# Performance work log

Hardware: AMD Instinct MI355X
Metric: run time of the kernel (lower is better)

The kernel has to match this reference:

```python
import jax, jax.numpy as jnp
import numpy as np

B, S, E, H = 4, 2048, 1024, 16
D = E // H


def setup_inputs() -> dict:
    key = jax.random.key(0)
    ks = jax.random.split(key, 4)
    scale = 0.02
    x = jax.random.normal(ks[0], (B, S, E), dtype=jnp.float32)
    in_proj_w = jax.random.normal(ks[1], (3 * E, E), dtype=jnp.float32) * scale
    in_proj_b = jnp.zeros((3 * E,), dtype=jnp.float32)
    out_w = jax.random.normal(ks[2], (E, E), dtype=jnp.float32) * scale
    out_b = jnp.zeros((E,), dtype=jnp.float32)
    rel_bias = jax.random.normal(ks[3], (2 * 32 + 1, H), dtype=jnp.float32) * 0.02
    return {"x": x, "in_proj_w": in_proj_w, "in_proj_b": in_proj_b,
            "out_w": out_w, "out_b": out_b, "rel_bias": rel_bias,
            "max_rel_dist": 32}


def reference(x, in_proj_w, in_proj_b, out_w, out_b, rel_bias, max_rel_dist):
    b, s, e = x.shape
    h = rel_bias.shape[1]
    d = e // h
    # relative-position indices, clamped: [S, S]
    i = jnp.arange(s)[:, None]
    j = jnp.arange(s)[None, :]
    rel = jnp.clip(i - j, -max_rel_dist, max_rel_dist) + max_rel_dist
    # gather per-pair per-head bias then average over heads -> single 2D mask
    attn_mask = jnp.mean(rel_bias[rel], axis=-1)  # [S, S]
    # fused QKV projection (PyTorch in_proj: x @ W^T + b)
    qkv = x @ in_proj_w.T + in_proj_b           # [B, S, 3E]
    q, k, v = jnp.split(qkv, 3, axis=-1)
    q = q.reshape(b, s, h, d)
    k = k.reshape(b, s, h, d)
    v = v.reshape(b, s, h, d)
    scale = 1.0 / jnp.sqrt(jnp.asarray(d, dtype=x.dtype))
    scores = jnp.einsum('bqhd,bkhd->bhqk', q, k) * scale + attn_mask  # [B,H,S,S]
    probs = jax.nn.softmax(scores, axis=-1)
    ctx = jnp.einsum('bhqk,bkhd->bqhd', probs, v).reshape(b, s, e)
    return ctx @ out_w.T + out_b
```

## Files before the change

kernel.cpp:

```cpp
#include <hip/hip_runtime.h>
#include <math.h>

#define B_ 4
#define S_ 2048
#define E_ 1024
#define H_ 16
#define D_ 64
#define MRD 32

typedef __bf16 bf16x8 __attribute__((ext_vector_type(8)));
typedef float f32x4 __attribute__((ext_vector_type(4)));
typedef float f32x16 __attribute__((ext_vector_type(16)));
typedef unsigned short us8 __attribute__((ext_vector_type(8)));
typedef unsigned short us4 __attribute__((ext_vector_type(4)));

union frag_cvt { us8 u; bf16x8 b; };
union h_cvt { __bf16 h; unsigned short u; };

__device__ __forceinline__ unsigned short bhi(float x) {
    h_cvt c; c.h = (__bf16)x; return c.u;
}
__device__ __forceinline__ float bf16_f(unsigned short h) {
    union { unsigned int u; float f; } c;
    c.u = ((unsigned int)h) << 16;
    return c.f;
}

__device__ __forceinline__ void async_copy16(const void* g, void* l) {
    __builtin_amdgcn_global_load_lds(
        (const __attribute__((address_space(1))) void*)g,
        (__attribute__((address_space(3))) void*)l,
        16, 0, 0);
}

__device__ __forceinline__ f32x16 mf32(const frag_cvt& a, const frag_cvt& b, f32x16 c) {
    return __builtin_amdgcn_mfma_f32_32x32x16_bf16(a.b, b.b, c, 0, 0, 0);
}

#define QSCL 0.18033688f
#define L2E  1.44269504f

__global__ __launch_bounds__(128) void cvt_bf16(
    const float* __restrict__ in, unsigned short* __restrict__ out, int K)
{
    const int r  = blockIdx.x;
    const int k8 = threadIdx.x * 8;
    if (k8 >= K) return;
    const float* p = in + (size_t)r * K + k8;
    float4 a = *(const float4*)p;
    float4 b = *(const float4*)(p + 4);
    float xs[8] = {a.x, a.y, a.z, a.w, b.x, b.y, b.z, b.w};
    us8 hu;
#pragma unroll
    for (int j = 0; j < 8; ++j) hu[j] = bhi(xs[j]);
    const int pos = (k8 & ~31) + ((((k8 >> 3) & 3) ^ (r & 3)) * 8);
    *(us8*)&out[(size_t)r * K + pos] = hu;
}

__global__ __launch_bounds__(128) void split_hilo(
    const float* __restrict__ in, unsigned short* __restrict__ out, int K)
{
    const int r  = blockIdx.x;
    const int k8 = threadIdx.x * 8;
    if (k8 >= K) return;
    const float* p = in + (size_t)r * K + k8;
    float4 a = *(const float4*)p;
    float4 b = *(const float4*)(p + 4);
    float xs[8] = {a.x, a.y, a.z, a.w, b.x, b.y, b.z, b.w};
    us8 hu, lu;
#pragma unroll
    for (int j = 0; j < 8; ++j) {
        unsigned short hb = bhi(xs[j]);
        hu[j] = hb;
        lu[j] = bhi(xs[j] - bf16_f(hb));
    }
    const int pos = (k8 & ~31) + ((((k8 >> 3) & 3) ^ (r & 3)) * 8);
    *(us8*)&out[(size_t)r * 2 * K + pos]     = hu;
    *(us8*)&out[(size_t)r * 2 * K + K + pos] = lu;
}

__global__ __launch_bounds__(256, 2) void gemm_qkv5(
    const unsigned short* __restrict__ Ab, const unsigned short* __restrict__ Bb,
    const float* __restrict__ bias, unsigned short* __restrict__ Qb,
    unsigned short* __restrict__ K2, unsigned short* __restrict__ Vt2,
    int M, int N, int K)
{
    __shared__ unsigned short At[128 * 32];
    __shared__ unsigned short Bt[128 * 32];

    const int t    = threadIdx.x;
    const int w    = t >> 6;
    const int lane = t & 63;
    const int ln   = lane & 15;
    const int quad = lane >> 4;
    const int wm   = w >> 1;
    const int wn   = w & 1;
    const int m0   = blockIdx.x * 128;
    const int n0   = blockIdx.y * 128;

    const int srow = w * 16 + (lane >> 2);
    const int scol = (lane & 3) * 8;
    const unsigned short* Abase = Ab + (size_t)(m0 + srow) * K + scol;
    const unsigned short* Bbase = Bb + (size_t)(n0 + srow) * K + scol;
    const int wlds = (w * 16) * 32;
    const int fro  = (quad ^ (ln & 3)) * 8;

    f32x4 acc[4][4];
#pragma unroll
    for (int i = 0; i < 4; ++i)
#pragma unroll
        for (int j = 0; j < 4; ++j)
            acc[i][j] = (f32x4){0.f, 0.f, 0.f, 0.f};

    for (int kk = 0; kk < K; kk += 32) {
        __syncthreads();
#pragma unroll
        for (int c = 0; c < 2; ++c) {
            const size_t ro = (size_t)(c * 64) * K;
            const int lo = c * 64 * 32 + wlds;
            async_copy16(Abase + ro + kk, &At[lo]);
            async_copy16(Bbase + ro + kk, &Bt[lo]);
        }
        __syncthreads();

        frag_cvt ah[4], bh[4];
#pragma unroll
        for (int i = 0; i < 4; ++i) {
            ah[i].u = *(const us8*)&At[(wm * 64 + i * 16 + ln) * 32 + fro];
            bh[i].u = *(const us8*)&Bt[(wn * 64 + i * 16 + ln) * 32 + fro];
        }
#pragma unroll
        for (int i = 0; i < 4; ++i)
#pragma unroll
            for (int j = 0; j < 4; ++j)
                acc[i][j] = __builtin_amdgcn_mfma_f32_16x16x32_bf16(
                    ah[i].b, bh[j].b, acc[i][j], 0, 0, 0);
    }

    if (n0 < E_) {
#pragma unroll
        for (int j = 0; j < 4; ++j) {
            const int col = n0 + wn * 64 + j * 16 + ln;
            const float bv = bias[col];
            const int h = (col & (E_ - 1)) >> 6, d = col & 63;
#pragma unroll
            for (int i = 0; i < 4; ++i) {
#pragma unroll
                for (int r = 0; r < 4; ++r) {
                    const int row = m0 + wm * 64 + i * 16 + quad * 4 + r;
                    const int b = row >> 11, s = row & (S_ - 1);
                    Qb[((size_t)(b * 16 + h) * S_ + s) * 64 + d] =
                        bhi((acc[i][j][r] + bv) * QSCL);
                }
            }
        }
    } else if (n0 < 2 * E_) {
#pragma unroll
        for (int j = 0; j < 4; ++j) {
            const int col = n0 + wn * 64 + j * 16 + ln;
            const float bv = bias[col];
            const int h = (col & (E_ - 1)) >> 6, d = col & 63;
#pragma unroll
            for (int i = 0; i < 4; ++i) {
#pragma unroll
                for (int r = 0; r < 4; ++r) {
                    const int row = m0 + wm * 64 + i * 16 + quad * 4 + r;
                    const int b = row >> 11, s = row & (S_ - 1);
                    K2[((size_t)(b * 16 + h) * S_ + s) * 64 +
                       (((d >> 3) ^ (s & 7)) * 8) + (d & 7)] =
                        bhi(acc[i][j][r] + bv);
                }
            }
        }
    } else {
#pragma unroll
        for (int j = 0; j < 4; ++j) {
            const int col = n0 + wn * 64 + j * 16 + ln;
            const float bv = bias[col];
            const int h = (col & (E_ - 1)) >> 6, d = col & 63;
#pragma unroll
            for (int i = 0; i < 4; ++i) {
                const int row0 = m0 + wm * 64 + i * 16 + quad * 4;
                const int b = row0 >> 11, s0 = row0 & (S_ - 1);
                const int tile = s0 >> 6;
                const int g = (s0 >> 3) & 7;
                us4 o;
#pragma unroll
                for (int r = 0; r < 4; ++r) o[r] = bhi(acc[i][j][r] + bv);
                *(us4*)&Vt2[(size_t)(b * 16 + h) * S_ * 64 + tile * 4096 +
                            d * 64 + ((g ^ (d & 7)) * 8) + (quad & 1) * 4] = o;
            }
        }
    }
}

__global__ __launch_bounds__(256, 3) void attn_mfma6(
    const unsigned short* __restrict__ Qb, const unsigned short* __restrict__ K2,
    const unsigned short* __restrict__ Vt2, const float* __restrict__ rel_bias,
    unsigned short* __restrict__ ctx2)
{
    __shared__ unsigned short Kt[2][4096];
    __shared__ unsigned short Vt[2][4096];
    __shared__ float bias_s[65];

    const int t    = threadIdx.x;
    const int w    = t >> 6;
    const int lane = t & 63;
    const int l31  = lane & 31;
    const int h    = lane >> 5;
    const int swzk = lane & 7;

    const int bh = blockIdx.x;
    const int b  = bh >> 4;
    const int hh = bh & 15;
    const int q0 = blockIdx.y * 128;

    if (t < 65) {
        float s = 0.f;
#pragma unroll
        for (int j = 0; j < 16; ++j) s += rel_bias[t * 16 + j];
        bias_s[t] = s * (L2E / 16.f);
    }

    frag_cvt qf[4];
    {
        const unsigned short* qp =
            Qb + ((size_t)bh * S_ + q0 + w * 32 + l31) * 64 + h * 8;
#pragma unroll
        for (int ks = 0; ks < 4; ++ks) qf[ks].u = *(const us8*)(qp + ks * 16);
    }

    frag_cvt ones;
#pragma unroll
    for (int j = 0; j < 8; ++j) ones.u[j] = 0x3F80;

    f32x16 Z;
#pragma unroll
    for (int i = 0; i < 16; ++i) Z[i] = 0.f;
    f32x16 O0 = Z, O1 = Z, lacc = Z;

    const unsigned short* Kg = K2  + (size_t)bh * S_ * 64;
    const unsigned short* Vg = Vt2 + (size_t)bh * S_ * 64;

    {
        const int uo = w * 512;
        async_copy16(Kg + uo + lane * 8,        &Kt[0][uo]);
        async_copy16(Kg + 2048 + uo + lane * 8, &Kt[0][2048 + uo]);
        async_copy16(Vg + uo + lane * 8,        &Vt[0][uo]);
        async_copy16(Vg + 2048 + uo + lane * 8, &Vt[0][2048 + uo]);
    }
    __syncthreads();

    for (int kt0 = 0; kt0 < 32; ++kt0) {
        const int cur = kt0 & 1;
        const int k0  = kt0 * 64;

        if (kt0 + 1 < 32) {
            const unsigned short* kg = Kg + (size_t)(k0 + 64) * 64;
            const unsigned short* vg = Vg + (size_t)(k0 + 64) * 64;
            unsigned short* kd = Kt[cur ^ 1];
            unsigned short* vd = Vt[cur ^ 1];
            const int uo = w * 512;
            async_copy16(kg + uo + lane * 8,        kd + uo);
            async_copy16(kg + 2048 + uo + lane * 8, kd + 2048 + uo);
            async_copy16(vg + uo + lane * 8,        vd + uo);
            async_copy16(vg + 2048 + uo + lane * 8, vd + 2048 + uo);
        }

        f32x16 sa0 = Z, sa1 = Z;
#pragma unroll
        for (int ks = 0; ks < 4; ++ks) {
            frag_cvt kh0, kh1;
            const int go = ((ks * 2 + h) ^ swzk) * 8;
            kh0.u = *(const us8*)&Kt[cur][l31 * 64 + go];
            kh1.u = *(const us8*)&Kt[cur][(32 + l31) * 64 + go];
            sa0 = mf32(kh0, qf[ks], sa0);
            sa1 = mf32(kh1, qf[ks], sa1);
        }

        const bool inband = (k0 >= q0 - 64) && (k0 <= q0 + 128);
        float cb = 0.f;
        if (!inband) cb = bias_s[(k0 < q0) ? 64 : 0];
        const int q = q0 + w * 32 + l31;

        unsigned int Wd[2][4][2];
#pragma unroll
        for (int kt = 0; kt < 2; ++kt) {
#pragma unroll
            for (int B2 = 0; B2 < 4; ++B2) {
#pragma unroll
                for (int p = 0; p < 2; ++p) {
                    unsigned int word = 0;
#pragma unroll
                    for (int rp = 0; rp < 2; ++rp) {
                        const int reg = B2 * 4 + p * 2 + rp;
                        const float sv = (kt == 0) ? sa0[reg] : sa1[reg];
                        float s2;
                        if (inband) {
                            const int key = k0 + kt * 32 + B2 * 8 + h * 4 + p * 2 + rp;
                            int rel = q - key;
                            rel = (rel < -MRD) ? -MRD : (rel > MRD ? MRD : rel);
                            s2 = sv + bias_s[rel + MRD];
                        } else {
                            s2 = sv + cb;
                        }
                        const float e = __builtin_amdgcn_exp2f(s2);
                        word |= ((unsigned int)bhi(e)) << (16 * rp);
                    }
                    Wd[kt][B2][p] = word;
                }
            }
        }

#pragma unroll
        for (int m = 0; m < 4; ++m) {
            const int kt  = m >> 1;
            const int sel = (m & 1) * 2;
            auto r0 = __builtin_amdgcn_permlane32_swap(
                Wd[kt][sel][0], Wd[kt][sel + 1][0], false, false);
            auto r1 = __builtin_amdgcn_permlane32_swap(
                Wd[kt][sel][1], Wd[kt][sel + 1][1], false, false);
            frag_cvt pa;
            union { us8 v; unsigned int d[4]; } uu;
            uu.d[0] = (unsigned int)r0[0];
            uu.d[1] = (unsigned int)r1[0];
            uu.d[2] = (unsigned int)r0[1];
            uu.d[3] = (unsigned int)r1[1];
            pa.u = uu.v;

            lacc = mf32(pa, ones, lacc);

            const int gv = ((m * 2 + h) ^ swzk) * 8;
            frag_cvt v0, v1;
            v0.u = *(const us8*)&Vt[cur][l31 * 64 + gv];
            v1.u = *(const us8*)&Vt[cur][(32 + l31) * 64 + gv];
            O0 = mf32(pa, v0, O0);
            O1 = mf32(pa, v1, O1);
        }

        __syncthreads();
    }

    float invq[16];
#pragma unroll
    for (int reg = 0; reg < 16; ++reg)
        invq[reg] = 1.f / lacc[reg];

#pragma unroll
    for (int dblk = 0; dblk < 2; ++dblk) {
#pragma unroll
        for (int reg = 0; reg < 16; ++reg) {
            const int qrow = q0 + w * 32 + (reg & 3) + 8 * (reg >> 2) + 4 * h;
            const float v = ((dblk == 0) ? O0[reg] : O1[reg]) * invq[reg];
            const unsigned short hb = bhi(v);
            const int k = hh * 64 + dblk * 32 + l31;
            const int pos = (k & ~31) + (((l31 >> 3) ^ (reg & 3)) * 8) + (k & 7);
            const size_t rb = (size_t)(b * S_ + qrow) * (2 * E_);
            ctx2[rb + pos]      = hb;
            ctx2[rb + E_ + pos] = bhi(v - bf16_f(hb));
        }
    }
}

__global__ __launch_bounds__(256, 2) void gemm_out4(
    const unsigned short* __restrict__ A2, const unsigned short* __restrict__ B2,
    const float* __restrict__ bias, float* __restrict__ C,
    int M, int N, int K)
{
    __shared__ unsigned short Ath[128 * 32], Atl[128 * 32];
    __shared__ unsigned short Bth[128 * 32], Btl[128 * 32];

    const int t    = threadIdx.x;
    const int w    = t >> 6;
    const int lane = t & 63;
    const int ln   = lane & 15;
    const int quad = lane >> 4;
    const int wm   = w >> 1;
    const int wn   = w & 1;
    const int m0   = blockIdx.x * 128;
    const int n0   = blockIdx.y * 128;
    const int K2s  = 2 * K;

    const int srow = w * 16 + (lane >> 2);
    const int scol = (lane & 3) * 8;
    const unsigned short* Abase = A2 + (size_t)(m0 + srow) * K2s + scol;
    const unsigned short* Bbase = B2 + (size_t)(n0 + srow) * K2s + scol;
    const int wlds = (w * 16) * 32;
    const int fro  = (quad ^ (ln & 3)) * 8;

    f32x4 acc[4][4];
#pragma unroll
    for (int i = 0; i < 4; ++i)
#pragma unroll
        for (int j = 0; j < 4; ++j)
            acc[i][j] = (f32x4){0.f, 0.f, 0.f, 0.f};

    for (int kk = 0; kk < K; kk += 32) {
        __syncthreads();
#pragma unroll
        for (int c = 0; c < 2; ++c) {
            const size_t ro = (size_t)(c * 64) * K2s;
            const int lo = c * 64 * 32 + wlds;
            async_copy16(Abase + ro + kk,     &Ath[lo]);
            async_copy16(Abase + ro + K + kk, &Atl[lo]);
            async_copy16(Bbase + ro + kk,     &Bth[lo]);
            async_copy16(Bbase + ro + K + kk, &Btl[lo]);
        }
        __syncthreads();

        frag_cvt ah[4], al[4], bh[4], bl[4];
#pragma unroll
        for (int i = 0; i < 4; ++i) {
            const int ar = (wm * 64 + i * 16 + ln) * 32 + fro;
            const int br = (wn * 64 + i * 16 + ln) * 32 + fro;
            ah[i].u = *(const us8*)&Ath[ar];
            al[i].u = *(const us8*)&Atl[ar];
            bh[i].u = *(const us8*)&Bth[br];
            bl[i].u = *(const us8*)&Btl[br];
        }
#pragma unroll
        for (int i = 0; i < 4; ++i)
#pragma unroll
            for (int j = 0; j < 4; ++j) {
                acc[i][j] = __builtin_amdgcn_mfma_f32_16x16x32_bf16(
                    ah[i].b, bh[j].b, acc[i][j], 0, 0, 0);
                acc[i][j] = __builtin_amdgcn_mfma_f32_16x16x32_bf16(
                    ah[i].b, bl[j].b, acc[i][j], 0, 0, 0);
                acc[i][j] = __builtin_amdgcn_mfma_f32_16x16x32_bf16(
                    al[i].b, bh[j].b, acc[i][j], 0, 0, 0);
            }
    }

#pragma unroll
    for (int j = 0; j < 4; ++j) {
        const int col = n0 + wn * 64 + j * 16 + ln;
        const float bv = bias[col];
#pragma unroll
        for (int i = 0; i < 4; ++i) {
            const int row = m0 + wm * 64 + i * 16 + quad * 4;
#pragma unroll
            for (int r = 0; r < 4; ++r)
                C[(size_t)(row + r) * N + col] = acc[i][j][r] + bv;
        }
    }
}

extern "C" void kernel_launch(void* const* d_in, const int* in_sizes, int n_in,
                              void* d_out, int out_size, void* d_ws, size_t ws_size,
                              hipStream_t stream)
{
    const float* x         = (const float*)d_in[0];
    const float* in_proj_w = (const float*)d_in[1];
    const float* in_proj_b = (const float*)d_in[2];
    const float* out_w     = (const float*)d_in[3];
    const float* out_b     = (const float*)d_in[4];
    const float* rel_bias  = (const float*)d_in[5];
    float* out = (float*)d_out;

    const int M = B_ * S_;
    const size_t PH = (size_t)B_ * H_ * S_ * 64;

    unsigned short* Qb   = (unsigned short*)d_ws;
    unsigned short* K2   = Qb + PH;
    unsigned short* Vt2  = K2 + PH;
    unsigned short* A2c  = Vt2 + PH;
    unsigned short* Axb  = A2c + (size_t)M * 2 * E_;
    unsigned short* Wqkv = Axb + (size_t)M * E_;
    unsigned short* W2o  = Wqkv + (size_t)3 * E_ * E_;

    cvt_bf16<<<M,      128, 0, stream>>>(x,         Axb,  E_);
    cvt_bf16<<<3 * E_, 128, 0, stream>>>(in_proj_w, Wqkv, E_);

    {
        dim3 grid(M / 128, (3 * E_) / 128);
        gemm_qkv5<<<grid, 256, 0, stream>>>(Axb, Wqkv, in_proj_b, Qb, K2, Vt2,
                                            M, 3 * E_, E_);
    }
    {
        dim3 grid(B_ * H_, S_ / 128);
        attn_mfma6<<<grid, 256, 0, stream>>>(Qb, K2, Vt2, rel_bias, A2c);
    }
    split_hilo<<<E_, 128, 0, stream>>>(out_w, W2o, E_);
    {
        dim3 grid(M / 128, E_ / 128);
        gemm_out4<<<grid, 256, 0, stream>>>(A2c, W2o, out_b, out, M, E_, E_);
    }
}
```

Before: 320.1 us.

## Double attention block size to 256 queries and add XCD-aware GEMM tile swizzle

```diff
diff --git a/kernel.cpp b/kernel.cpp
--- a/kernel.cpp
+++ b/kernel.cpp
@@ -95,8 +95,13 @@
     const int quad = lane >> 4;
     const int wm   = w >> 1;
     const int wn   = w & 1;
-    const int m0   = blockIdx.x * 128;
-    const int n0   = blockIdx.y * 128;
+
+    const int nbx = gridDim.x, nby = gridDim.y;
+    int lin = blockIdx.x + blockIdx.y * nbx;
+    const int per = (nbx * nby) >> 3;
+    lin = (lin & 7) * per + (lin >> 3);
+    const int m0 = (lin / nby) * 128;
+    const int n0 = (lin % nby) * 128;
 
     const int srow = w * 16 + (lane >> 2);
     const int scol = (lane & 3) * 8;
@@ -194,7 +199,7 @@
     }
 }
 
-__global__ __launch_bounds__(256, 3) void attn_mfma6(
+__global__ __launch_bounds__(512, 4) void attn_mfma7(
     const unsigned short* __restrict__ Qb, const unsigned short* __restrict__ K2,
     const unsigned short* __restrict__ Vt2, const float* __restrict__ rel_bias,
     unsigned short* __restrict__ ctx2)
@@ -210,10 +215,11 @@
     const int h    = lane >> 5;
     const int swzk = lane & 7;
 
-    const int bh = blockIdx.x;
-    const int b  = bh >> 4;
-    const int hh = bh & 15;
-    const int q0 = blockIdx.y * 128;
+    const int bh  = blockIdx.x;
+    const int b   = bh >> 4;
+    const int hh  = bh & 15;
+    const int q0  = blockIdx.y * 256;
+    const int qw0 = q0 + w * 32;
 
     if (t < 65) {
         float s = 0.f;
@@ -225,7 +231,7 @@
     frag_cvt qf[4];
     {
         const unsigned short* qp =
-            Qb + ((size_t)bh * S_ + q0 + w * 32 + l31) * 64 + h * 8;
+            Qb + ((size_t)bh * S_ + qw0 + l31) * 64 + h * 8;
 #pragma unroll
         for (int ks = 0; ks < 4; ++ks) qf[ks].u = *(const us8*)(qp + ks * 16);
     }
@@ -243,11 +249,14 @@
     const unsigned short* Vg = Vt2 + (size_t)bh * S_ * 64;
 
     {
-        const int uo = w * 512;
-        async_copy16(Kg + uo + lane * 8,        &Kt[0][uo]);
-        async_copy16(Kg + 2048 + uo + lane * 8, &Kt[0][2048 + uo]);
-        async_copy16(Vg + uo + lane * 8,        &Vt[0][uo]);
-        async_copy16(Vg + 2048 + uo + lane * 8, &Vt[0][2048 + uo]);
+        const int seg = (w & 3) * 1024;
+        if (w < 4) {
+            async_copy16(Kg + seg + lane * 8,       &Kt[0][seg]);
+            async_copy16(Kg + seg + 512 + lane * 8, &Kt[0][seg + 512]);
+        } else {
+            async_copy16(Vg + seg + lane * 8,       &Vt[0][seg]);
+            async_copy16(Vg + seg + 512 + lane * 8, &Vt[0][seg + 512]);
+        }
     }
     __syncthreads();
 
@@ -258,13 +267,14 @@
         if (kt0 + 1 < 32) {
             const unsigned short* kg = Kg + (size_t)(k0 + 64) * 64;
             const unsigned short* vg = Vg + (size_t)(k0 + 64) * 64;
-            unsigned short* kd = Kt[cur ^ 1];
-            unsigned short* vd = Vt[cur ^ 1];
-            const int uo = w * 512;
-            async_copy16(kg + uo + lane * 8,        kd + uo);
-            async_copy16(kg + 2048 + uo + lane * 8, kd + 2048 + uo);
-            async_copy16(vg + uo + lane * 8,        vd + uo);
-            async_copy16(vg + 2048 + uo + lane * 8, vd + 2048 + uo);
+            const int seg = (w & 3) * 1024;
+            if (w < 4) {
+                async_copy16(kg + seg + lane * 8,       &Kt[cur ^ 1][seg]);
+                async_copy16(kg + seg + 512 + lane * 8, &Kt[cur ^ 1][seg + 512]);
+            } else {
+                async_copy16(vg + seg + lane * 8,       &Vt[cur ^ 1][seg]);
+                async_copy16(vg + seg + 512 + lane * 8, &Vt[cur ^ 1][seg + 512]);
+            }
         }
 
         f32x16 sa0 = Z, sa1 = Z;
@@ -278,10 +288,10 @@
             sa1 = mf32(kh1, qf[ks], sa1);
         }
 
-        const bool inband = (k0 >= q0 - 64) && (k0 <= q0 + 128);
+        const bool inband = (k0 >= qw0 - 95) && (k0 <= qw0 + 63);
         float cb = 0.f;
-        if (!inband) cb = bias_s[(k0 < q0) ? 64 : 0];
-        const int q = q0 + w * 32 + l31;
+        if (!inband) cb = bias_s[(k0 < qw0) ? 64 : 0];
+        const int q = qw0 + l31;
 
         unsigned int Wd[2][4][2];
 #pragma unroll
@@ -350,7 +360,7 @@
     for (int dblk = 0; dblk < 2; ++dblk) {
 #pragma unroll
         for (int reg = 0; reg < 16; ++reg) {
-            const int qrow = q0 + w * 32 + (reg & 3) + 8 * (reg >> 2) + 4 * h;
+            const int qrow = qw0 + (reg & 3) + 8 * (reg >> 2) + 4 * h;
             const float v = ((dblk == 0) ? O0[reg] : O1[reg]) * invq[reg];
             const unsigned short hb = bhi(v);
             const int k = hh * 64 + dblk * 32 + l31;
@@ -377,8 +387,14 @@
     const int quad = lane >> 4;
     const int wm   = w >> 1;
     const int wn   = w & 1;
-    const int m0   = blockIdx.x * 128;
-    const int n0   = blockIdx.y * 128;
+
+    const int nbx = gridDim.x, nby = gridDim.y;
+    int lin = blockIdx.x + blockIdx.y * nbx;
+    const int per = (nbx * nby) >> 3;
+    lin = (lin & 7) * per + (lin >> 3);
+    const int m0 = (lin / nby) * 128;
+    const int n0 = (lin % nby) * 128;
+
     const int K2s  = 2 * K;
 
     const int srow = w * 16 + (lane >> 2);
@@ -477,8 +493,8 @@
                                             M, 3 * E_, E_);
     }
     {
-        dim3 grid(B_ * H_, S_ / 128);
-        attn_mfma6<<<grid, 256, 0, stream>>>(Qb, K2, Vt2, rel_bias, A2c);
+        dim3 grid(B_ * H_, S_ / 256);
+        attn_mfma7<<<grid, 512, 0, stream>>>(Qb, K2, Vt2, rel_bias, A2c);
     }
     split_hilo<<<E_, 128, 0, stream>>>(out_w, W2o, E_);
     {
```

Result: slower. 350.8 us (+9.6%).
